# Kernel tuning notes

Measured on AMD Instinct MI355X. Metric: run time of the kernel, lower is better.

## Reference

```python
import jax, jax.numpy as jnp
import numpy as np

N, E = 50000, 800000
F_IN, F_OUT, H = 128, 16, 8
NEG_SLOPE = 0.2  # PyG GATConv default
EPS = 1e-5       # LayerNorm eps


def setup_inputs() -> dict:
    key = jax.random.key(0)
    ks = jax.random.split(key, 8)
    x = jax.random.normal(ks[0], (N, F_IN), dtype=jnp.float32)
    edge_index = jax.random.randint(ks[1], (2, E), 0, N, dtype=jnp.int32)
    s_in = 1.0 / np.sqrt(F_IN)
    s_f = 1.0 / np.sqrt(F_OUT)
    W = jax.random.normal(ks[2], (F_IN, H * F_OUT), dtype=jnp.float32) * s_in
    att_src = jax.random.normal(ks[3], (H, F_OUT), dtype=jnp.float32) * s_f
    att_dst = jax.random.normal(ks[4], (H, F_OUT), dtype=jnp.float32) * s_f
    bias = jnp.zeros((H * F_OUT,), dtype=jnp.float32)
    gamma = jnp.ones((H * F_OUT,), dtype=jnp.float32)
    beta = jnp.zeros((H * F_OUT,), dtype=jnp.float32)
    return {"x": x, "edge_index": edge_index, "W": W, "att_src": att_src,
            "att_dst": att_dst, "bias": bias, "gamma": gamma, "beta": beta}


def _gat_layer(x, edge_index, W, att_src, att_dst, bias, gamma, beta):
    n = x.shape[0]
    # add self loops (PyG GATConv default add_self_loops=True)
    loop = jnp.arange(n, dtype=edge_index.dtype)
    src = jnp.concatenate([edge_index[0], loop])  # message source j
    dst = jnp.concatenate([edge_index[1], loop])  # message target i

    xp = (x @ W).reshape(n, H, F_OUT)                      # [N,H,F]
    a_src = jnp.einsum('nhf,hf->nh', xp, att_src)          # [N,H]
    a_dst = jnp.einsum('nhf,hf->nh', xp, att_dst)          # [N,H]

    e = a_src[src] + a_dst[dst]                            # [E+N,H]
    e = jax.nn.leaky_relu(e, NEG_SLOPE)
    # softmax over incoming edges per destination node
    m = jax.ops.segment_max(e, dst, num_segments=n)        # [N,H]
    e = jnp.exp(e - m[dst])
    z = jax.ops.segment_sum(e, dst, num_segments=n)        # [N,H]
    alpha = e / jnp.where(z[dst] > 0, z[dst], 1.0)         # [E+N,H]

    msg = alpha[:, :, None] * xp[src]                      # [E+N,H,F]
    out = jax.ops.segment_sum(msg, dst, num_segments=n)    # [N,H,F]
    out = out.reshape(n, H * F_OUT) + bias

    # LayerNorm over feature dim
    mu = out.mean(axis=-1, keepdims=True)
    var = out.var(axis=-1, keepdims=True)
    return (out - mu) * jax.lax.rsqrt(var + EPS) * gamma + beta


def reference(x, edge_index, W, att_src, att_dst, bias, gamma, beta):
    return _gat_layer(x, edge_index, W, att_src, att_dst, bias, gamma, beta)
```

## Files before the change

kernel.cpp:

```cpp
#include <hip/hip_runtime.h>
#include <math.h>

#define F_IN 128
#define NHD 8
#define FEAT 128
#define NEG_SLOPE 0.2f
#define LN_EPS 1e-5f
#define BSH 7
#define BMSK 127
#define NPQ 32
#define CAP 48
#define EPB 2048
#define NBMAX 512

typedef __bf16 v8bf __attribute__((ext_vector_type(8)));
typedef __bf16 v2bf __attribute__((ext_vector_type(2)));
typedef float f32x4 __attribute__((ext_vector_type(4)));

__global__ __launch_bounds__(256) void k_wt(const float* __restrict__ W,
                                            __bf16* __restrict__ WT) {
    int idx = blockIdx.x * 256 + threadIdx.x;
    int k = idx >> 7, c = idx & 127;
    WT[c * 128 + k] = (__bf16)W[idx];
}

__global__ __launch_bounds__(512) void k_fused(const float* __restrict__ x,
                                               const __bf16* __restrict__ WT,
                                               const float* __restrict__ att_src,
                                               const float* __restrict__ att_dst,
                                               __bf16* __restrict__ xp16,
                                               float* __restrict__ a_src,
                                               float* __restrict__ a_dst,
                                               const int* __restrict__ src,
                                               const int* __restrict__ dst,
                                               unsigned int* __restrict__ sorted_g,
                                               int* __restrict__ runptr,
                                               int n, int E, int Ga) {
    __shared__ __bf16 xs[32][136];
    if ((int)blockIdx.x < Ga) {
        __shared__ int lcnt[NBMAX];
        __shared__ int loff[NBMAX + 1];
        __shared__ unsigned int sorted_l[EPB];
        __shared__ int wtot[8], wexcl[8];
        int NB = (n + BMSK) >> BSH;
        int tid = threadIdx.x, lane = tid & 63, wid = tid >> 6;
        long base0 = (long)blockIdx.x * EPB;
        long total = (long)E + n;
        if (tid < NB) lcnt[tid] = 0;
        __syncthreads();

        int s0[4], d0[4];
        bool val[4];
        long e0 = base0 + (long)tid * 4;
        if (e0 + 3 < E) {
            int4 sv = *(const int4*)(src + e0);
            int4 dv = *(const int4*)(dst + e0);
            s0[0] = sv.x; s0[1] = sv.y; s0[2] = sv.z; s0[3] = sv.w;
            d0[0] = dv.x; d0[1] = dv.y; d0[2] = dv.z; d0[3] = dv.w;
            val[0] = val[1] = val[2] = val[3] = true;
        } else {
#pragma unroll
            for (int j = 0; j < 4; ++j) {
                long e = e0 + j;
                val[j] = (e < total);
                s0[j] = d0[j] = 0;
                if (val[j]) {
                    if (e < E) { s0[j] = src[e]; d0[j] = dst[e]; }
                    else { s0[j] = d0[j] = (int)(e - E); }
                }
            }
        }
#pragma unroll
        for (int j = 0; j < 4; ++j)
            if (val[j]) atomicAdd(&lcnt[d0[j] >> BSH], 1);
        __syncthreads();

        int v = (tid < NB) ? lcnt[tid] : 0;
        int xx = v;
#pragma unroll
        for (int o = 1; o < 64; o <<= 1) {
            int t2 = __shfl_up(xx, o);
            if (lane >= o) xx += t2;
        }
        if (lane == 63) wtot[wid] = xx;
        __syncthreads();
        if (wid == 0 && lane < 8) {
            int s = wtot[lane];
            int y = s;
#pragma unroll
            for (int o = 1; o < 8; o <<= 1) {
                int t2 = __shfl_up(y, o);
                if (lane >= o) y += t2;
            }
            wexcl[lane] = y - s;
        }
        __syncthreads();
        int excl = wexcl[wid] + xx - v;
        if (tid < NB) loff[tid] = excl;
        if (tid == NB - 1) loff[NB] = excl + v;
        __syncthreads();
        if (tid < NB) lcnt[tid] = loff[tid];
        __syncthreads();
#pragma unroll
        for (int j = 0; j < 4; ++j) {
            if (val[j]) {
                int b = d0[j] >> BSH;
                int pos = atomicAdd(&lcnt[b], 1);
                sorted_l[pos] = ((unsigned)s0[j] << BSH) | (unsigned)(d0[j] & BMSK);
            }
        }
        __syncthreads();
        int tv = loff[NB];
        for (int i = tid; i < tv; i += 512)
            sorted_g[base0 + i] = sorted_l[i];
        if (tid <= NB) runptr[(long)blockIdx.x * (NBMAX + 1) + tid] = loff[tid];
    } else {
        int gb = blockIdx.x - Ga;
        int tid = threadIdx.x;
        int rowbase = gb * 32;
        {
            int i4 = tid;
#pragma unroll
            for (int rep = 0; rep < 2; ++rep, i4 += 512) {
                int r = i4 >> 5, c4 = i4 & 31;
                int gr = rowbase + r; if (gr > n - 1) gr = n - 1;
                float4 xv = *(const float4*)(x + (long)gr * 128 + c4 * 4);
                __bf16* p = &xs[r][c4 * 4];
                p[0] = (__bf16)xv.x; p[1] = (__bf16)xv.y;
                p[2] = (__bf16)xv.z; p[3] = (__bf16)xv.w;
            }
        }
        __syncthreads();
        int wv = tid >> 6;
        int lane = tid & 63;
        int m = lane & 15, quad = lane >> 4;
        int colbase = wv * 16;
        const __bf16* wcol = WT + (colbase + m) * 128;
        v8bf wf[4];
#pragma unroll
        for (int kk = 0; kk < 4; ++kk)
            wf[kk] = *(const v8bf*)(wcol + kk * 32 + quad * 8);
        float ws = att_src[colbase + m];
        float wd = att_dst[colbase + m];
#pragma unroll
        for (int t = 0; t < 2; ++t) {
            int rb = t * 16;
            f32x4 acc = {0.f, 0.f, 0.f, 0.f};
#pragma unroll
            for (int kk = 0; kk < 4; ++kk) {
                v8bf a = *(const v8bf*)(&xs[rb + m][kk * 32 + quad * 8]);
                acc = __builtin_amdgcn_mfma_f32_16x16x32_bf16(a, wf[kk], acc, 0, 0, 0);
            }
#pragma unroll
            for (int r = 0; r < 4; ++r) {
                int row = rowbase + rb + quad * 4 + r;
                float ts = acc[r] * ws;
                float td = acc[r] * wd;
#pragma unroll
                for (int o = 1; o < 16; o <<= 1) {
                    ts += __shfl_xor(ts, o);
                    td += __shfl_xor(td, o);
                }
                if (row < n) {
                    xp16[(long)row * 128 + colbase + m] = (__bf16)acc[r];
                    if (m == 0) {
                        a_src[row * 8 + wv] = ts;
                        a_dst[row * 8 + wv] = td;
                    }
                }
            }
        }
    }
}

__global__ __launch_bounds__(256) void k_ba(const unsigned int* __restrict__ sorted_g,
                                            const int* __restrict__ runptr,
                                            const float* __restrict__ a_src,
                                            const float* __restrict__ a_dst,
                                            const __bf16* __restrict__ xp16,
                                            const float* __restrict__ bias,
                                            const float* __restrict__ gamma,
                                            const float* __restrict__ beta,
                                            const int* __restrict__ src,
                                            const int* __restrict__ dst,
                                            float* __restrict__ out, int n, int E, int Ga) {
    __shared__ int slds[NPQ * CAP];
    __shared__ int lc[NPQ];
    __shared__ float adst_s[NPQ * NHD];
    int b = blockIdx.x >> 2;
    int q = blockIdx.x & 3;
    int tid = threadIdx.x;
    int node0 = (b << BSH) + q * NPQ;
    if (tid < NPQ) lc[tid] = 0;
    if (tid < NPQ * NHD) {
        int nd = node0 + (tid >> 3);
        adst_s[tid] = (nd < n) ? a_dst[nd * NHD + (tid & 7)] : 0.f;
    }
    __syncthreads();

    int qlo = q * NPQ;
    for (int blk = tid; blk < Ga; blk += 256) {
        const int* rp = runptr + (long)blk * (NBMAX + 1) + b;
        int st = rp[0], en = rp[1];
        const unsigned int* sg = sorted_g + (long)blk * EPB;
        for (int i = st; i < en; ++i) {
            unsigned int u = sg[i];
            int dl = (int)(u & BMSK) - qlo;
            if ((unsigned)dl < NPQ) {
                int p = atomicAdd(&lc[dl], 1);
                if (p < CAP) slds[dl * CAP + p] = (int)(u >> BSH);
            }
        }
    }
    __syncthreads();
    if (tid < NPQ) {
        int cc = lc[tid]; if (cc > CAP) cc = CAP;
        int pad = (cc + 7) & ~7; if (pad > CAP) pad = CAP;
        for (int p = cc; p < pad; ++p) slds[tid * CAP + p] = 0;
    }
    __syncthreads();

    int lane = tid & 63, wv = tid >> 6;
    int h = lane & 7, j8 = lane >> 3;
    float2 bs = *(const float2*)(bias + 2 * lane);
    float2 g  = *(const float2*)(gamma + 2 * lane);
    float2 bt = *(const float2*)(beta + 2 * lane);

    for (int i = wv; i < NPQ; i += 4) {
        int node = node0 + i;
        if (node >= n) break;
        int cnt = lc[i];
        float acc0 = 0.f, acc1 = 0.f, inv;

        if (cnt <= CAP) {
            const int* row = slds + i * CAP;
            float b_h = adst_s[i * NHD + h];
            float zacc = 0.f;
            for (int base = 0; base < cnt; base += 8) {
                int s_my = row[base + j8];
                float e = a_src[s_my * NHD + h] + b_h;
                e = e > 0.f ? e : NEG_SLOPE * e;
                float w_my = (base + j8 < cnt) ? __expf(e) : 0.f;
                zacc += w_my;
                int ss[8];
#pragma unroll
                for (int j = 0; j < 8; ++j) ss[j] = row[base + j];
                float2 vals[8];
#pragma unroll
                for (int j = 0; j < 8; ++j) {
                    v2bf p = *(const v2bf*)(xp16 + (long)ss[j] * FEAT + 2 * lane);
                    vals[j] = make_float2((float)p[0], (float)p[1]);
                }
#pragma unroll
                for (int j = 0; j < 8; ++j) {
                    float w = __shfl(w_my, j * 8 + j8);
                    acc0 = fmaf(w, vals[j].x, acc0);
                    acc1 = fmaf(w, vals[j].y, acc1);
                }
            }
            zacc += __shfl_xor(zacc, 8);
            zacc += __shfl_xor(zacc, 16);
            zacc += __shfl_xor(zacc, 32);
            float z = __shfl(zacc, j8);
            inv = 1.f / z;
        } else {
            float b_h = a_dst[node * NHD + j8];
            float z = 0.f;
            {
                float e = a_src[node * NHD + j8] + b_h;
                e = e > 0.f ? e : NEG_SLOPE * e;
                float w = __expf(e);
                z += w;
                v2bf p = *(const v2bf*)(xp16 + (long)node * FEAT + 2 * lane);
                acc0 = fmaf(w, (float)p[0], acc0);
                acc1 = fmaf(w, (float)p[1], acc1);
            }
            for (int base = 0; base < E; base += 64) {
                int e = base + lane;
                int sv = 0;
                bool mt = false;
                if (e < E) { mt = (dst[e] == node); if (mt) sv = src[e]; }
                unsigned long long mask = __ballot(mt);
                while (mask) {
                    int bl = __ffsll(mask) - 1;
                    mask &= mask - 1;
                    int s = __shfl(sv, bl);
                    float ee = a_src[s * NHD + j8] + b_h;
                    ee = ee > 0.f ? ee : NEG_SLOPE * ee;
                    float w = __expf(ee);
                    z += w;
                    v2bf p = *(const v2bf*)(xp16 + (long)s * FEAT + 2 * lane);
                    acc0 = fmaf(w, (float)p[0], acc0);
                    acc1 = fmaf(w, (float)p[1], acc1);
                }
            }
            inv = 1.f / z;
        }

        float v0 = acc0 * inv + bs.x;
        float v1 = acc1 * inv + bs.y;
        float ssum = v0 + v1;
        float ssq = v0 * v0 + v1 * v1;
#pragma unroll
        for (int o = 32; o > 0; o >>= 1) {
            ssum += __shfl_xor(ssum, o);
            ssq += __shfl_xor(ssq, o);
        }
        float mu = ssum * (1.0f / FEAT);
        float var = ssq * (1.0f / FEAT) - mu * mu;
        float rs = rsqrtf(var + LN_EPS);
        float2 o2;
        o2.x = (v0 - mu) * rs * g.x + bt.x;
        o2.y = (v1 - mu) * rs * g.y + bt.y;
        *(float2*)(out + (long)node * FEAT + 2 * lane) = o2;
    }
}

extern "C" void kernel_launch(void* const* d_in, const int* in_sizes, int n_in,
                              void* d_out, int out_size, void* d_ws, size_t ws_size,
                              hipStream_t stream) {
    const float* x = (const float*)d_in[0];
    const int* edge_index = (const int*)d_in[1];
    const float* W = (const float*)d_in[2];
    const float* att_src = (const float*)d_in[3];
    const float* att_dst = (const float*)d_in[4];
    const float* bias = (const float*)d_in[5];
    const float* gamma = (const float*)d_in[6];
    const float* beta = (const float*)d_in[7];
    float* out = (float*)d_out;

    int n = in_sizes[0] / F_IN;
    int E = in_sizes[1] / 2;
    const int* src = edge_index;
    const int* dst = edge_index + E;
    int NB = (n + BMSK) >> BSH;
    int Ga = (E + n + EPB - 1) / EPB;

    char* ws = (char*)d_ws;
    __bf16* WT   = (__bf16*)ws;                    ws += (size_t)128 * 128 * 2;
    __bf16* xp16 = (__bf16*)ws;                    ws += (size_t)n * FEAT * 2;
    float* a_src = (float*)ws;                     ws += (size_t)n * NHD * 4;
    float* a_dst = (float*)ws;                     ws += (size_t)n * NHD * 4;
    unsigned int* sorted_g = (unsigned int*)ws;    ws += (size_t)Ga * EPB * 4;
    int* runptr  = (int*)ws;                       ws += (size_t)Ga * (NBMAX + 1) * 4;

    k_wt<<<64, 256, 0, stream>>>(W, WT);
    int Gg = (n + 31) / 32;
    k_fused<<<Ga + Gg, 512, 0, stream>>>(x, WT, att_src, att_dst, xp16, a_src, a_dst,
                                         src, dst, sorted_g, runptr, n, E, Ga);
    k_ba<<<NB * 4, 256, 0, stream>>>(sorted_g, runptr, a_src, a_dst, xp16,
                                     bias, gamma, beta, src, dst, out, n, E, Ga);
}
```

Measured before the change: 179.6 us.

## Add bucket reorder pass, fold attention vectors into GEMM, halve nodes per block

```diff
diff --git a/kernel.cpp b/kernel.cpp
--- a/kernel.cpp
+++ b/kernel.cpp
@@ -8,26 +8,44 @@
 #define LN_EPS 1e-5f
 #define BSH 7
 #define BMSK 127
-#define NPQ 32
+#define NPQ 16
 #define CAP 48
 #define EPB 2048
 #define NBMAX 512
+#define BCAP 6144
+#define WCOLS 144
 
 typedef __bf16 v8bf __attribute__((ext_vector_type(8)));
 typedef __bf16 v2bf __attribute__((ext_vector_type(2)));
 typedef float f32x4 __attribute__((ext_vector_type(4)));
 
 __global__ __launch_bounds__(256) void k_wt(const float* __restrict__ W,
+                                            const float* __restrict__ att_src,
+                                            const float* __restrict__ att_dst,
                                             __bf16* __restrict__ WT) {
     int idx = blockIdx.x * 256 + threadIdx.x;
-    int k = idx >> 7, c = idx & 127;
-    WT[c * 128 + k] = (__bf16)W[idx];
+    int c = idx >> 7, k = idx & 127;
+    float v;
+    if (c < 128) {
+        v = W[k * 128 + c];
+    } else if (c < 136) {
+        int h = c - 128;
+        float s = 0.f;
+#pragma unroll
+        for (int f = 0; f < 16; ++f) s += W[k * 128 + h * 16 + f] * att_src[h * 16 + f];
+        v = s;
+    } else {
+        int h = c - 136;
+        float s = 0.f;
+#pragma unroll
+        for (int f = 0; f < 16; ++f) s += W[k * 128 + h * 16 + f] * att_dst[h * 16 + f];
+        v = s;
+    }
+    WT[c * 128 + k] = (__bf16)v;
 }
 
 __global__ __launch_bounds__(512) void k_fused(const float* __restrict__ x,
                                                const __bf16* __restrict__ WT,
-                                               const float* __restrict__ att_src,
-                                               const float* __restrict__ att_dst,
                                                __bf16* __restrict__ xp16,
                                                float* __restrict__ a_src,
                                                float* __restrict__ a_dst,
@@ -36,7 +54,7 @@
                                                unsigned int* __restrict__ sorted_g,
                                                int* __restrict__ runptr,
                                                int n, int E, int Ga) {
-    __shared__ __bf16 xs[32][136];
+    __shared__ __bf16 xs[64][136];
     if ((int)blockIdx.x < Ga) {
         __shared__ int lcnt[NBMAX];
         __shared__ int loff[NBMAX + 1];
@@ -117,11 +135,11 @@
     } else {
         int gb = blockIdx.x - Ga;
         int tid = threadIdx.x;
-        int rowbase = gb * 32;
+        int rowbase = gb * 64;
         {
             int i4 = tid;
 #pragma unroll
-            for (int rep = 0; rep < 2; ++rep, i4 += 512) {
+            for (int rep = 0; rep < 4; ++rep, i4 += 512) {
                 int r = i4 >> 5, c4 = i4 & 31;
                 int gr = rowbase + r; if (gr > n - 1) gr = n - 1;
                 float4 xv = *(const float4*)(x + (long)gr * 128 + c4 * 4);
@@ -140,10 +158,15 @@
 #pragma unroll
         for (int kk = 0; kk < 4; ++kk)
             wf[kk] = *(const v8bf*)(wcol + kk * 32 + quad * 8);
-        float ws = att_src[colbase + m];
-        float wd = att_dst[colbase + m];
-#pragma unroll
-        for (int t = 0; t < 2; ++t) {
+        v8bf wf2[4];
+        if (wv < 4) {
+            const __bf16* wcol2 = WT + (128 + m) * 128;
+#pragma unroll
+            for (int kk = 0; kk < 4; ++kk)
+                wf2[kk] = *(const v8bf*)(wcol2 + kk * 32 + quad * 8);
+        }
+#pragma unroll
+        for (int t = 0; t < 4; ++t) {
             int rb = t * 16;
             f32x4 acc = {0.f, 0.f, 0.f, 0.f};
 #pragma unroll
@@ -154,27 +177,77 @@
 #pragma unroll
             for (int r = 0; r < 4; ++r) {
                 int row = rowbase + rb + quad * 4 + r;
-                float ts = acc[r] * ws;
-                float td = acc[r] * wd;
-#pragma unroll
-                for (int o = 1; o < 16; o <<= 1) {
-                    ts += __shfl_xor(ts, o);
-                    td += __shfl_xor(td, o);
+                if (row < n)
+                    xp16[(long)row * 128 + colbase + m] = (__bf16)acc[r];
+            }
+        }
+        if (wv < 4) {
+            int rb = wv * 16;
+            f32x4 acc = {0.f, 0.f, 0.f, 0.f};
+#pragma unroll
+            for (int kk = 0; kk < 4; ++kk) {
+                v8bf a = *(const v8bf*)(&xs[rb + m][kk * 32 + quad * 8]);
+                acc = __builtin_amdgcn_mfma_f32_16x16x32_bf16(a, wf2[kk], acc, 0, 0, 0);
+            }
+#pragma unroll
+            for (int r = 0; r < 4; ++r) {
+                int row = rowbase + rb + quad * 4 + r;
+                if (row < n) {
+                    if (m < 8) a_src[row * 8 + m] = acc[r];
+                    else       a_dst[row * 8 + (m - 8)] = acc[r];
                 }
-                if (row < n) {
-                    xp16[(long)row * 128 + colbase + m] = (__bf16)acc[r];
-                    if (m == 0) {
-                        a_src[row * 8 + wv] = ts;
-                        a_dst[row * 8 + wv] = td;
-                    }
-                }
             }
         }
     }
 }
 
-__global__ __launch_bounds__(256) void k_ba(const unsigned int* __restrict__ sorted_g,
-                                            const int* __restrict__ runptr,
+__global__ __launch_bounds__(256) void k_reorder(const unsigned int* __restrict__ sorted_g,
+                                                 const int* __restrict__ runptr,
+                                                 unsigned int* __restrict__ sorted2,
+                                                 int* __restrict__ bcnt, int Ga) {
+    int b = blockIdx.x;
+    int tid = threadIdx.x, lane = tid & 63, wid = tid >> 6;
+    __shared__ int wsum[4], wexcl_s[4];
+    __shared__ int carry_s;
+    if (tid == 0) carry_s = 0;
+    __syncthreads();
+    for (int base = 0; base < Ga; base += 256) {
+        int blk = base + tid;
+        int st = 0, c = 0;
+        if (blk < Ga) {
+            const int* rp = runptr + (long)blk * (NBMAX + 1) + b;
+            st = rp[0];
+            c = rp[1] - st;
+        }
+        int xx = c;
+#pragma unroll
+        for (int o = 1; o < 64; o <<= 1) {
+            int t2 = __shfl_up(xx, o);
+            if (lane >= o) xx += t2;
+        }
+        if (lane == 63) wsum[wid] = xx;
+        __syncthreads();
+        if (tid == 0) {
+            int s = 0;
+#pragma unroll
+            for (int w = 0; w < 4; ++w) { wexcl_s[w] = s; s += wsum[w]; }
+            wsum[0] = s;
+        }
+        __syncthreads();
+        int excl = carry_s + wexcl_s[wid] + xx - c;
+        const unsigned int* sg = sorted_g + (long)blk * EPB + st;
+        unsigned int* dp = sorted2 + (long)b * BCAP + excl;
+        int lim = BCAP - excl;
+        for (int i = 0; i < c && i < lim; ++i) dp[i] = sg[i];
+        __syncthreads();
+        if (tid == 0) carry_s += wsum[0];
+        __syncthreads();
+    }
+    if (tid == 0) bcnt[b] = carry_s < BCAP ? carry_s : BCAP;
+}
+
+__global__ __launch_bounds__(256) void k_ba(const unsigned int* __restrict__ sorted2,
+                                            const int* __restrict__ bcnt,
                                             const float* __restrict__ a_src,
                                             const float* __restrict__ a_dst,
                                             const __bf16* __restrict__ xp16,
@@ -183,12 +256,12 @@
                                             const float* __restrict__ beta,
                                             const int* __restrict__ src,
                                             const int* __restrict__ dst,
-                                            float* __restrict__ out, int n, int E, int Ga) {
+                                            float* __restrict__ out, int n, int E) {
     __shared__ int slds[NPQ * CAP];
     __shared__ int lc[NPQ];
     __shared__ float adst_s[NPQ * NHD];
-    int b = blockIdx.x >> 2;
-    int q = blockIdx.x & 3;
+    int b = blockIdx.x >> 3;
+    int q = blockIdx.x & 7;
     int tid = threadIdx.x;
     int node0 = (b << BSH) + q * NPQ;
     if (tid < NPQ) lc[tid] = 0;
@@ -198,18 +271,15 @@
     }
     __syncthreads();
 
+    int cnt_b = bcnt[b];
+    const unsigned int* sg = sorted2 + (long)b * BCAP;
     int qlo = q * NPQ;
-    for (int blk = tid; blk < Ga; blk += 256) {
-        const int* rp = runptr + (long)blk * (NBMAX + 1) + b;
-        int st = rp[0], en = rp[1];
-        const unsigned int* sg = sorted_g + (long)blk * EPB;
-        for (int i = st; i < en; ++i) {
-            unsigned int u = sg[i];
-            int dl = (int)(u & BMSK) - qlo;
-            if ((unsigned)dl < NPQ) {
-                int p = atomicAdd(&lc[dl], 1);
-                if (p < CAP) slds[dl * CAP + p] = (int)(u >> BSH);
-            }
+    for (int i = tid; i < cnt_b; i += 256) {
+        unsigned int u = sg[i];
+        int dl = (int)(u & BMSK) - qlo;
+        if ((unsigned)dl < (unsigned)NPQ) {
+            int p = atomicAdd(&lc[dl], 1);
+            if (p < CAP) slds[dl * CAP + p] = (int)(u >> BSH);
         }
     }
     __syncthreads();
@@ -335,19 +405,22 @@
     const int* dst = edge_index + E;
     int NB = (n + BMSK) >> BSH;
     int Ga = (E + n + EPB - 1) / EPB;
+    int Gg = (n + 63) / 64;
 
     char* ws = (char*)d_ws;
-    __bf16* WT   = (__bf16*)ws;                    ws += (size_t)128 * 128 * 2;
+    __bf16* WT   = (__bf16*)ws;                    ws += (size_t)WCOLS * 128 * 2;
     __bf16* xp16 = (__bf16*)ws;                    ws += (size_t)n * FEAT * 2;
     float* a_src = (float*)ws;                     ws += (size_t)n * NHD * 4;
     float* a_dst = (float*)ws;                     ws += (size_t)n * NHD * 4;
     unsigned int* sorted_g = (unsigned int*)ws;    ws += (size_t)Ga * EPB * 4;
+    unsigned int* sorted2 = (unsigned int*)ws;     ws += (size_t)NB * BCAP * 4;
+    int* bcnt = (int*)ws;                          ws += (size_t)NB * 4;
     int* runptr  = (int*)ws;                       ws += (size_t)Ga * (NBMAX + 1) * 4;
 
-    k_wt<<<64, 256, 0, stream>>>(W, WT);
-    int Gg = (n + 31) / 32;
-    k_fused<<<Ga + Gg, 512, 0, stream>>>(x, WT, att_src, att_dst, xp16, a_src, a_dst,
+    k_wt<<<72, 256, 0, stream>>>(W, att_src, att_dst, WT);
+    k_fused<<<Ga + Gg, 512, 0, stream>>>(x, WT, xp16, a_src, a_dst,
                                          src, dst, sorted_g, runptr, n, E, Ga);
-    k_ba<<<NB * 4, 256, 0, stream>>>(sorted_g, runptr, a_src, a_dst, xp16,
-                                     bias, gamma, beta, src, dst, out, n, E, Ga);
+    k_reorder<<<NB, 256, 0, stream>>>(sorted_g, runptr, sorted2, bcnt, Ga);
+    k_ba<<<NB * 8, 256, 0, stream>>>(sorted2, bcnt, a_src, a_dst, xp16,
+                                     bias, gamma, beta, src, dst, out, n, E);
 }
```

Result: faster. 165.5 us (-7.9%).
